# Kernel tuning notes

Hardware: AMD Instinct MI355X
Metric: run time of the kernel (lower is better)

Reference implementation:

```python
import jax, jax.numpy as jnp
import numpy as np

N = 50000      # nodes
E = 800000     # edges (avg degree 16)
H = 128        # hidden
ED = 64        # edge_dim
L = 3          # num_layers
LN_EPS = 1e-5


def setup_inputs() -> dict:
    key = jax.random.key(0)
    ks = jax.random.split(key, 12)
    s = jax.random.normal(ks[0], (N, H), dtype=jnp.float32)
    edge_index = jax.random.randint(ks[1], (2, E), 0, N, dtype=jnp.int32)
    edge_attr = jax.random.normal(ks[2], (E, ED), dtype=jnp.float32)
    sc = 0.02
    We = sc * jax.random.normal(ks[3], (L, ED, H), dtype=jnp.float32)
    be = sc * jax.random.normal(ks[4], (L, H), dtype=jnp.float32)
    W1 = sc * jax.random.normal(ks[5], (L, H, H), dtype=jnp.float32)
    b1 = sc * jax.random.normal(ks[6], (L, H), dtype=jnp.float32)
    W2 = sc * jax.random.normal(ks[7], (L, H, H), dtype=jnp.float32)
    b2 = sc * jax.random.normal(ks[8], (L, H), dtype=jnp.float32)
    gamma = jnp.ones((L, H), dtype=jnp.float32)
    beta = jnp.zeros((L, H), dtype=jnp.float32)
    return {"s": s, "edge_index": edge_index, "edge_attr": edge_attr,
            "We": We, "be": be, "W1": W1, "b1": b1, "W2": W2, "b2": b2,
            "gamma": gamma, "beta": beta}


def reference(s, edge_index, edge_attr, We, be, W1, b1, W2, b2, gamma, beta):
    src = edge_index[0]  # j (source of message)
    dst = edge_index[1]  # i (target / aggregation index)
    for l in range(L):
        # GINEConv: message = relu(x_j + Lin(edge_attr)); sum-aggregate; eps=0
        e = edge_attr @ We[l] + be[l]                       # [E, H]
        msg = jax.nn.relu(s[src] + e)                       # [E, H] gather + fuse
        agg = jax.ops.segment_sum(msg, dst, num_segments=N)  # [N, H] scatter-add
        h = s + agg                                         # (1+eps)*x + aggr, eps=0
        h = jax.nn.silu(h @ W1[l] + b1[l]) @ W2[l] + b2[l]   # GINE MLP
        s = s + h                                           # residual
        mu = jnp.mean(s, axis=-1, keepdims=True)
        var = jnp.var(s, axis=-1, keepdims=True)
        s = (s - mu) * jax.lax.rsqrt(var + LN_EPS) * gamma[l] + beta[l]
        s = jax.nn.silu(s)
        # dropout p=0.0 / eval mode -> identity
    return s
```

## Files before the change

kernel.cpp:

```cpp
#include <hip/hip_runtime.h>
#include <hip/hip_bf16.h>

#define HH 128
#define EDD 64
#define NLAYER 3
#define LN_EPS 1e-5f
#define LROW 136

typedef __attribute__((ext_vector_type(8))) __bf16 bf16x8;
typedef __attribute__((ext_vector_type(4))) float f32x4;

static __device__ __forceinline__ float bf2f(unsigned short u) {
    return __uint_as_float(((unsigned)u) << 16);
}
static __device__ __forceinline__ unsigned short f2bf(float f) {
    return __builtin_bit_cast(unsigned short, (__bf16)f);
}
static __device__ __forceinline__ float silu(float x) {
    return x / (1.f + __expf(-x));
}

__global__ __launch_bounds__(256) void hist_kernel(
    const int* __restrict__ dst, int* __restrict__ cnt, int E)
{
    for (int e = blockIdx.x * blockDim.x + threadIdx.x; e < E;
         e += gridDim.x * blockDim.x)
        atomicAdd(&cnt[dst[e]], 1);
}

__global__ __launch_bounds__(1024) void scan_kernel(
    const int* __restrict__ cnt, int* __restrict__ off, int N)
{
    __shared__ int ls[1024];
    const int t = threadIdx.x;
    const int C = (N + 1023) >> 10;
    const int lo = t * C;
    const int hi = min(lo + C, N);
    int sum = 0;
    for (int i = lo; i < hi; ++i) sum += cnt[i];
    ls[t] = sum;
    __syncthreads();
    for (int d = 1; d < 1024; d <<= 1) {
        int v = (t >= d) ? ls[t - d] : 0;
        __syncthreads();
        ls[t] += v;
        __syncthreads();
    }
    int excl = (t == 0) ? 0 : ls[t - 1];
    for (int i = lo; i < hi; ++i) { off[i] = excl; excl += cnt[i]; }
    if (t == 1023) off[N] = ls[1023];
}

__global__ __launch_bounds__(256) void scatter2_kernel(
    const int* __restrict__ src, const int* __restrict__ dst,
    int* __restrict__ cursor, int* __restrict__ src_s,
    int* __restrict__ eid_s, int E)
{
    if (blockIdx.x == 0 && threadIdx.x < 16) {
        src_s[E + threadIdx.x] = 0;
        eid_s[E + threadIdx.x] = 0;
    }
    for (int e = blockIdx.x * blockDim.x + threadIdx.x; e < E;
         e += gridDim.x * blockDim.x) {
        const int pos = atomicAdd(&cursor[dst[e]], 1);
        src_s[pos] = src[e];
        eid_s[pos] = e;
    }
}

__global__ __launch_bounds__(256) void conv_ea(
    const float* __restrict__ ea, unsigned short* __restrict__ ea_b,
    long long total4)
{
    for (long long i = blockIdx.x * 256LL + threadIdx.x; i < total4;
         i += gridDim.x * 256LL) {
        const float4 v = reinterpret_cast<const float4*>(ea)[i];
        ushort4 o;
        o.x = f2bf(v.x); o.y = f2bf(v.y); o.z = f2bf(v.z); o.w = f2bf(v.w);
        reinterpret_cast<ushort4*>(ea_b)[i] = o;
    }
}

__global__ __launch_bounds__(256) void conv_s(
    const float* __restrict__ s0, unsigned int* __restrict__ sbp,
    long long total4)
{
    for (long long i = blockIdx.x * 256LL + threadIdx.x; i < total4;
         i += gridDim.x * 256LL) {
        const float4 v = reinterpret_cast<const float4*>(s0)[i];
        const unsigned a = (unsigned)f2bf(v.x) | ((unsigned)f2bf(v.y) << 16);
        const unsigned b = (unsigned)f2bf(v.z) | ((unsigned)f2bf(v.w) << 16);
        reinterpret_cast<uint2*>(sbp)[i] = make_uint2(a, b);
    }
}

__global__ void prep_we(const float* __restrict__ We, bf16x8* __restrict__ WeB)
{
    const int t = blockIdx.x * blockDim.x + threadIdx.x;
    if (t >= NLAYER * 16 * 64) return;
    const int lane  = t & 63;
    const int frag  = (t >> 6) & 15;
    const int layer = t >> 10;
    const int kt = frag >> 3, ct = frag & 7;
    const int col = ct * 16 + (lane & 15);
    const int k0  = kt * 32 + (lane >> 4) * 8;
    bf16x8 v;
    #pragma unroll
    for (int j = 0; j < 8; ++j)
        v[j] = (__bf16)We[(long long)layer * EDD * HH + (k0 + j) * HH + col];
    WeB[t] = v;
}

__global__ void prep_w128(const float* __restrict__ W, bf16x8* __restrict__ WB)
{
    const int t = blockIdx.x * blockDim.x + threadIdx.x;
    if (t >= NLAYER * 32 * 64) return;
    const int lane  = t & 63;
    const int frag  = (t >> 6) & 31;
    const int layer = t >> 11;
    const int kt = frag >> 3, ct = frag & 7;
    const int col = ct * 16 + (lane & 15);
    const int k0  = kt * 32 + (lane >> 4) * 8;
    bf16x8 v;
    #pragma unroll
    for (int j = 0; j < 8; ++j)
        v[j] = (__bf16)W[(long long)layer * HH * HH + (k0 + j) * HH + col];
    WB[t] = v;
}

__global__ __launch_bounds__(256) void gine_agg_mfma(
    const float* __restrict__ s,
    const unsigned short* __restrict__ sb,
    const int* __restrict__ src_s,
    const int* __restrict__ eid_s,
    const int* __restrict__ off,
    const unsigned short* __restrict__ ea_b,
    const bf16x8* __restrict__ WeB,
    const float* __restrict__ be,
    unsigned short* __restrict__ hb16,
    int N, int E)
{
    __shared__ unsigned short lsb[2][16 * LROW];

    const int tid  = threadIdx.x;
    const int wave = tid >> 6;
    const int half = wave & 1;
    const int slot = wave >> 1;
    const int lane = tid & 63;
    const int lmod = lane & 15;
    const int ldiv = lane >> 4;

    bf16x8 wb0[4], wb1[4];
    #pragma unroll
    for (int c = 0; c < 4; ++c) {
        wb0[c] = WeB[(0 * 8 + half * 4 + c) * 64 + lane];
        wb1[c] = WeB[(1 * 8 + half * 4 + c) * 64 + lane];
    }
    float bev[4];
    #pragma unroll
    for (int c = 0; c < 4; ++c) bev[c] = be[(half * 4 + c) * 16 + lmod];

    const int st_slot = tid >> 7;
    const int st_row  = (tid >> 3) & 15;
    const int st_sp   = tid & 7;

    for (int base = blockIdx.x * 2; base < N; base += gridDim.x * 2) {
        const int n0 = base;
        const int n1 = (base + 1 < N) ? base + 1 : base;
        const int q0 = off[n0], q0e = off[n0 + 1];
        const int q1 = off[n1], q1e = off[n1 + 1];
        const int iters = max((q0e - q0 + 15) >> 4, (q1e - q1 + 15) >> 4);

        const int myn = slot ? n1 : n0;
        const int p0  = slot ? q1 : q0;
        const int p1  = slot ? q1e : q0e;
        const int sp0 = st_slot ? q1 : q0;

        float acc[4] = {0.f, 0.f, 0.f, 0.f};

        for (int it = 0; it < iters; ++it) {
            const int sidx  = min(sp0 + it * 16 + st_row, E + 15);
            const int snode = src_s[sidx];
            const unsigned short* srow = &sb[(long long)snode * HH + st_sp * 16];
            const uint4 sva = *reinterpret_cast<const uint4*>(srow);
            const uint4 svb = *reinterpret_cast<const uint4*>(srow + 8);

            __syncthreads();
            unsigned short* drow = &lsb[st_slot][st_row * LROW + st_sp * 16];
            *reinterpret_cast<uint4*>(drow)     = sva;
            *reinterpret_cast<uint4*>(drow + 8) = svb;

            const int p   = p0 + it * 16;
            const int rem = p1 - p;
            const int rowid = eid_s[min(p + lmod, E + 15)];
            const unsigned short* arow = ea_b + (long long)rowid * EDD + ldiv * 8;
            const bf16x8 a0 = *reinterpret_cast<const bf16x8*>(arow);
            const bf16x8 a1 = *reinterpret_cast<const bf16x8*>(arow + 32);

            f32x4 cf[4];
            #pragma unroll
            for (int c = 0; c < 4; ++c) {
                f32x4 z = {0.f, 0.f, 0.f, 0.f};
                z = __builtin_amdgcn_mfma_f32_16x16x32_bf16(a0, wb0[c], z, 0, 0, 0);
                z = __builtin_amdgcn_mfma_f32_16x16x32_bf16(a1, wb1[c], z, 0, 0, 0);
                cf[c] = z;
            }

            __syncthreads();

            #pragma unroll
            for (int r = 0; r < 4; ++r) {
                if (ldiv * 4 + r < rem) {
                    const unsigned short* lr = &lsb[slot][(ldiv * 4 + r) * LROW];
                    #pragma unroll
                    for (int c = 0; c < 4; ++c) {
                        acc[c] += fmaxf(
                            bf2f(lr[(half * 4 + c) * 16 + lmod]) + cf[c][r] + bev[c],
                            0.f);
                    }
                }
            }
        }

        #pragma unroll
        for (int c = 0; c < 4; ++c) {
            acc[c] += __shfl_xor(acc[c], 16, 64);
            acc[c] += __shfl_xor(acc[c], 32, 64);
        }
        const float av = (ldiv == 0) ? acc[0] : (ldiv == 1) ? acc[1]
                       : (ldiv == 2) ? acc[2] : acc[3];
        const int col = (half * 4 + ldiv) * 16 + lmod;
        const long long nb = (long long)myn * HH;
        hb16[nb + col] = f2bf(s[nb + col] + av);
    }
}

__global__ __launch_bounds__(256) void gine_mlp(
    const float* __restrict__ s_in,
    const unsigned short* __restrict__ h16,
    const bf16x8* __restrict__ W1B, const float* __restrict__ b1,
    const bf16x8* __restrict__ W2B, const float* __restrict__ b2,
    const float* __restrict__ gamma, const float* __restrict__ beta,
    float* __restrict__ s_out,
    unsigned short* __restrict__ sb_out,
    int N)
{
    __shared__ unsigned short t1t[16 * LROW];
    __shared__ float2 red[4][16];

    const int wave = threadIdx.x >> 6;
    const int lane = threadIdx.x & 63;
    const int lmod = lane & 15;
    const int ldiv = lane >> 4;

    bf16x8 wf1[4][2], wf2[4][2];
    #pragma unroll
    for (int kt = 0; kt < 4; ++kt) {
        wf1[kt][0] = W1B[(kt * 8 + 2 * wave    ) * 64 + lane];
        wf1[kt][1] = W1B[(kt * 8 + 2 * wave + 1) * 64 + lane];
        wf2[kt][0] = W2B[(kt * 8 + 2 * wave    ) * 64 + lane];
        wf2[kt][1] = W2B[(kt * 8 + 2 * wave + 1) * 64 + lane];
    }
    float4 b1v[2], b2v[2], gv[2], ev[2];
    #pragma unroll
    for (int ctl = 0; ctl < 2; ++ctl) {
        const int oc0 = (2 * wave + ctl) * 16 + ldiv * 4;
        b1v[ctl] = *reinterpret_cast<const float4*>(&b1[oc0]);
        b2v[ctl] = *reinterpret_cast<const float4*>(&b2[oc0]);
        gv[ctl]  = *reinterpret_cast<const float4*>(&gamma[oc0]);
        ev[ctl]  = *reinterpret_cast<const float4*>(&beta[oc0]);
    }

    const int ntiles = (N + 15) >> 4;
    for (int t = blockIdx.x; t < ntiles; t += gridDim.x) {
        const int node = t * 16 + lmod;
        const long long nb = (long long)min(node, N - 1) * HH;

        f32x4 c0 = {0.f, 0.f, 0.f, 0.f};
        f32x4 c1 = {0.f, 0.f, 0.f, 0.f};
        #pragma unroll
        for (int kt = 0; kt < 4; ++kt) {
            const bf16x8 hf = *reinterpret_cast<const bf16x8*>(
                &h16[nb + kt * 32 + ldiv * 8]);
            c0 = __builtin_amdgcn_mfma_f32_16x16x32_bf16(wf1[kt][0], hf, c0, 0, 0, 0);
            c1 = __builtin_amdgcn_mfma_f32_16x16x32_bf16(wf1[kt][1], hf, c1, 0, 0, 0);
        }
        #pragma unroll
        for (int ctl = 0; ctl < 2; ++ctl) {
            const f32x4 cc = ctl ? c1 : c0;
            const float4 bb = ctl ? b1v[1] : b1v[0];
            uint2 pk;
            pk.x = (unsigned)f2bf(silu(cc[0] + bb.x)) |
                   ((unsigned)f2bf(silu(cc[1] + bb.y)) << 16);
            pk.y = (unsigned)f2bf(silu(cc[2] + bb.z)) |
                   ((unsigned)f2bf(silu(cc[3] + bb.w)) << 16);
            const int oc0 = (2 * wave + ctl) * 16 + ldiv * 4;
            *reinterpret_cast<uint2*>(&t1t[lmod * LROW + oc0]) = pk;
        }
        __syncthreads();

        f32x4 d0 = {0.f, 0.f, 0.f, 0.f};
        f32x4 d1 = {0.f, 0.f, 0.f, 0.f};
        #pragma unroll
        for (int kt = 0; kt < 4; ++kt) {
            const bf16x8 tf = *reinterpret_cast<const bf16x8*>(
                &t1t[lmod * LROW + kt * 32 + ldiv * 8]);
            d0 = __builtin_amdgcn_mfma_f32_16x16x32_bf16(wf2[kt][0], tf, d0, 0, 0, 0);
            d1 = __builtin_amdgcn_mfma_f32_16x16x32_bf16(wf2[kt][1], tf, d1, 0, 0, 0);
        }

        float v[2][4];
        float sum = 0.f, ssq = 0.f;
        #pragma unroll
        for (int ctl = 0; ctl < 2; ++ctl) {
            const int oc0 = (2 * wave + ctl) * 16 + ldiv * 4;
            const float4 sv = *reinterpret_cast<const float4*>(&s_in[nb + oc0]);
            const f32x4 dd = ctl ? d1 : d0;
            const float4 bb = ctl ? b2v[1] : b2v[0];
            v[ctl][0] = sv.x + dd[0] + bb.x;
            v[ctl][1] = sv.y + dd[1] + bb.y;
            v[ctl][2] = sv.z + dd[2] + bb.z;
            v[ctl][3] = sv.w + dd[3] + bb.w;
            #pragma unroll
            for (int r = 0; r < 4; ++r) { sum += v[ctl][r]; ssq += v[ctl][r] * v[ctl][r]; }
        }
        sum += __shfl_xor(sum, 16, 64); sum += __shfl_xor(sum, 32, 64);
        ssq += __shfl_xor(ssq, 16, 64); ssq += __shfl_xor(ssq, 32, 64);
        if (ldiv == 0) red[wave][lmod] = make_float2(sum, ssq);
        __syncthreads();
        float ts = 0.f, tq = 0.f;
        #pragma unroll
        for (int w = 0; w < 4; ++w) {
            const float2 rr = red[w][lmod];
            ts += rr.x; tq += rr.y;
        }
        __syncthreads();

        const float mu = ts * (1.0f / HH);
        const float var = tq * (1.0f / HH) - mu * mu;
        const float rs = rsqrtf(var + LN_EPS);

        if (node < N) {
            #pragma unroll
            for (int ctl = 0; ctl < 2; ++ctl) {
                const int oc0 = (2 * wave + ctl) * 16 + ldiv * 4;
                float o[4];
                o[0] = silu((v[ctl][0] - mu) * rs * gv[ctl].x + ev[ctl].x);
                o[1] = silu((v[ctl][1] - mu) * rs * gv[ctl].y + ev[ctl].y);
                o[2] = silu((v[ctl][2] - mu) * rs * gv[ctl].z + ev[ctl].z);
                o[3] = silu((v[ctl][3] - mu) * rs * gv[ctl].w + ev[ctl].w);
                *reinterpret_cast<float4*>(&s_out[nb + oc0]) =
                    make_float4(o[0], o[1], o[2], o[3]);
                uint2 pk;
                pk.x = (unsigned)f2bf(o[0]) | ((unsigned)f2bf(o[1]) << 16);
                pk.y = (unsigned)f2bf(o[2]) | ((unsigned)f2bf(o[3]) << 16);
                *reinterpret_cast<uint2*>(&sb_out[nb + oc0]) = pk;
            }
        }
    }
}

extern "C" void kernel_launch(void* const* d_in, const int* in_sizes, int n_in,
                              void* d_out, int out_size, void* d_ws, size_t ws_size,
                              hipStream_t stream) {
    const float* s0  = (const float*)d_in[0];
    const int*   ei  = (const int*)  d_in[1];
    const float* ea  = (const float*)d_in[2];
    const float* We  = (const float*)d_in[3];
    const float* be  = (const float*)d_in[4];
    const float* W1  = (const float*)d_in[5];
    const float* b1  = (const float*)d_in[6];
    const float* W2  = (const float*)d_in[7];
    const float* b2  = (const float*)d_in[8];
    const float* gm  = (const float*)d_in[9];
    const float* bt  = (const float*)d_in[10];

    const int NH = in_sizes[0];
    const int N  = NH / HH;
    const int E  = in_sizes[1] / 2;
    const int* src = ei;
    const int* dst = ei + E;

    float*          sbuf  = (float*)d_ws;
    unsigned short* sb    = (unsigned short*)(sbuf + NH);
    unsigned short* hb16  = sb + NH;
    unsigned short* ea_b  = hb16 + NH;
    bf16x8*         WeB   = (bf16x8*)(ea_b + (size_t)E * EDD);
    bf16x8*         W1B   = WeB + NLAYER * 16 * 64;
    bf16x8*         W2B   = W1B + NLAYER * 32 * 64;
    int*            src_s = (int*)(W2B + NLAYER * 32 * 64);
    int*            eid_s = src_s + (E + 16);
    int*            off   = eid_s + (E + 16);
    int*            cursor= off + (N + 1);

    hipMemcpyAsync(sbuf, s0, sizeof(float) * NH, hipMemcpyDeviceToDevice, stream);

    hipMemsetAsync(cursor, 0, sizeof(int) * N, stream);
    hist_kernel<<<1024, 256, 0, stream>>>(dst, cursor, E);
    scan_kernel<<<1, 1024, 0, stream>>>(cursor, off, N);
    hipMemcpyAsync(cursor, off, sizeof(int) * N, hipMemcpyDeviceToDevice, stream);
    scatter2_kernel<<<1024, 256, 0, stream>>>(src, dst, cursor, src_s, eid_s, E);
    conv_ea<<<2048, 256, 0, stream>>>(ea, ea_b, (long long)E * EDD / 4);
    conv_s<<<1024, 256, 0, stream>>>(s0, (unsigned int*)sb, (long long)NH / 4);
    prep_we<<<12, 256, 0, stream>>>(We, WeB);
    prep_w128<<<24, 256, 0, stream>>>(W1, W1B);
    prep_w128<<<24, 256, 0, stream>>>(W2, W2B);

    for (int l = 0; l < NLAYER; ++l) {
        gine_agg_mfma<<<4096, 256, 0, stream>>>(sbuf, sb, src_s, eid_s, off, ea_b,
                                                WeB + (size_t)l * 16 * 64,
                                                be + l * HH, hb16, N, E);
        float* sout = (l == NLAYER - 1) ? (float*)d_out : sbuf;
        gine_mlp<<<2048, 256, 0, stream>>>(sbuf, hb16,
                                           W1B + (size_t)l * 32 * 64, b1 + l * HH,
                                           W2B + (size_t)l * 32 * 64, b2 + l * HH,
                                           gm + l * HH, bt + l * HH,
                                           sout, sb, N);
    }
}
```

Before: 652.4 us.

## Software-pipeline gather loads in aggregation kernel and drop initial state copy

Restructures the aggregation loop so the next iteration's source-node rows and edge-attribute rows are loaded into registers before the current iteration's MFMA and accumulate work, hiding global gather latency. Adds a launch-bounds occupancy hint of 3 blocks per CU. Also removes the initial device-to-device copy of s by reading layer 0 directly from the input buffer. The prefetch raises register pressure, which the occupancy hint may either constrain or turn into spills.

```diff
diff --git a/kernel.cpp b/kernel.cpp
--- a/kernel.cpp
+++ b/kernel.cpp
@@ -128,7 +128,7 @@
     WB[t] = v;
 }
 
-__global__ __launch_bounds__(256) void gine_agg_mfma(
+__global__ __launch_bounds__(256, 3) void gine_agg_mfma(
     const float* __restrict__ s,
     const unsigned short* __restrict__ sb,
     const int* __restrict__ src_s,
@@ -162,7 +162,7 @@
 
     const int st_slot = tid >> 7;
     const int st_row  = (tid >> 3) & 15;
-    const int st_sp   = tid & 7;
+    const int st_su   = (tid & 7) * 16;
 
     for (int base = blockIdx.x * 2; base < N; base += gridDim.x * 2) {
         const int n0 = base;
@@ -178,24 +178,33 @@
 
         float acc[4] = {0.f, 0.f, 0.f, 0.f};
 
+        int snode = src_s[min(sp0 + st_row, E + 15)];
+        const unsigned short* srow0 = &sb[(long long)snode * HH + st_su];
+        uint4 sva = *reinterpret_cast<const uint4*>(srow0);
+        uint4 svb = *reinterpret_cast<const uint4*>(srow0 + 8);
+        int rowid = eid_s[min(p0 + lmod, E + 15)];
+        const unsigned short* ar0 = ea_b + (long long)rowid * EDD + ldiv * 8;
+        bf16x8 a0 = *reinterpret_cast<const bf16x8*>(ar0);
+        bf16x8 a1 = *reinterpret_cast<const bf16x8*>(ar0 + 32);
+
         for (int it = 0; it < iters; ++it) {
-            const int sidx  = min(sp0 + it * 16 + st_row, E + 15);
-            const int snode = src_s[sidx];
-            const unsigned short* srow = &sb[(long long)snode * HH + st_sp * 16];
-            const uint4 sva = *reinterpret_cast<const uint4*>(srow);
-            const uint4 svb = *reinterpret_cast<const uint4*>(srow + 8);
-
             __syncthreads();
-            unsigned short* drow = &lsb[st_slot][st_row * LROW + st_sp * 16];
+            unsigned short* drow = &lsb[st_slot][st_row * LROW + st_su];
             *reinterpret_cast<uint4*>(drow)     = sva;
             *reinterpret_cast<uint4*>(drow + 8) = svb;
 
-            const int p   = p0 + it * 16;
-            const int rem = p1 - p;
-            const int rowid = eid_s[min(p + lmod, E + 15)];
-            const unsigned short* arow = ea_b + (long long)rowid * EDD + ldiv * 8;
-            const bf16x8 a0 = *reinterpret_cast<const bf16x8*>(arow);
-            const bf16x8 a1 = *reinterpret_cast<const bf16x8*>(arow + 32);
+            uint4 nva = sva, nvb = svb;
+            bf16x8 na0 = a0, na1 = a1;
+            if (it + 1 < iters) {
+                const int ns = src_s[min(sp0 + (it + 1) * 16 + st_row, E + 15)];
+                const unsigned short* nsr = &sb[(long long)ns * HH + st_su];
+                nva = *reinterpret_cast<const uint4*>(nsr);
+                nvb = *reinterpret_cast<const uint4*>(nsr + 8);
+                const int nr = eid_s[min(p0 + (it + 1) * 16 + lmod, E + 15)];
+                const unsigned short* nar = ea_b + (long long)nr * EDD + ldiv * 8;
+                na0 = *reinterpret_cast<const bf16x8*>(nar);
+                na1 = *reinterpret_cast<const bf16x8*>(nar + 32);
+            }
 
             f32x4 cf[4];
             #pragma unroll
@@ -208,18 +217,20 @@
 
             __syncthreads();
 
+            const int rem = p1 - (p0 + it * 16);
             #pragma unroll
             for (int r = 0; r < 4; ++r) {
                 if (ldiv * 4 + r < rem) {
                     const unsigned short* lr = &lsb[slot][(ldiv * 4 + r) * LROW];
                     #pragma unroll
-                    for (int c = 0; c < 4; ++c) {
+                    for (int c = 0; c < 4; ++c)
                         acc[c] += fmaxf(
                             bf2f(lr[(half * 4 + c) * 16 + lmod]) + cf[c][r] + bev[c],
                             0.f);
-                    }
                 }
             }
+
+            sva = nva; svb = nvb; a0 = na0; a1 = na1;
         }
 
         #pragma unroll
@@ -393,8 +404,6 @@
     int*            off   = eid_s + (E + 16);
     int*            cursor= off + (N + 1);
 
-    hipMemcpyAsync(sbuf, s0, sizeof(float) * NH, hipMemcpyDeviceToDevice, stream);
-
     hipMemsetAsync(cursor, 0, sizeof(int) * N, stream);
     hist_kernel<<<1024, 256, 0, stream>>>(dst, cursor, E);
     scan_kernel<<<1, 1024, 0, stream>>>(cursor, off, N);
@@ -407,11 +416,12 @@
     prep_w128<<<24, 256, 0, stream>>>(W2, W2B);
 
     for (int l = 0; l < NLAYER; ++l) {
-        gine_agg_mfma<<<4096, 256, 0, stream>>>(sbuf, sb, src_s, eid_s, off, ea_b,
+        const float* scur = (l == 0) ? s0 : sbuf;
+        gine_agg_mfma<<<4096, 256, 0, stream>>>(scur, sb, src_s, eid_s, off, ea_b,
                                                 WeB + (size_t)l * 16 * 64,
                                                 be + l * HH, hb16, N, E);
         float* sout = (l == NLAYER - 1) ? (float*)d_out : sbuf;
-        gine_mlp<<<2048, 256, 0, stream>>>(sbuf, hb16,
+        gine_mlp<<<2048, 256, 0, stream>>>(scur, hb16,
                                            W1B + (size_t)l * 32 * 64, b1 + l * HH,
                                            W2B + (size_t)l * 32 * 64, b2 + l * HH,
                                            gm + l * HH, bt + l * HH,
```

Result: faster. 611.8 us (-6.2%).
